# Performance work log

Hardware: AMD Instinct MI355X
Metric: run time of the kernel (lower is better)

Reference implementation:

```python
import jax, jax.numpy as jnp
import numpy as np

CHEB_K = 3


def _cheb(support):
    # Chebyshev polynomial basis [I, A, 2A@T_{k-1} - T_{k-2}] of a dense (N,N) support
    N = support.shape[0]
    ks = [jnp.eye(N, dtype=support.dtype), support]
    for _ in range(2, CHEB_K):
        ks.append(2.0 * support @ ks[-1] - ks[-2])
    return ks


def _agcn(x, sk, W, b):
    # x: (B,N,C); sk: list of (N,N); W: (2*cheb_k*C, O)
    xg = jnp.concatenate([jnp.einsum('nm,bmc->bnc', s, x) for s in sk], axis=-1)
    return jnp.einsum('bni,io->bno', xg, W) + b


def _cell(x, h, sk, Wg, bg, Wu, bu):
    # adaptive graph-conv GRU cell
    hd = h.shape[-1]
    zr = jax.nn.sigmoid(_agcn(jnp.concatenate([x, h], axis=-1), sk, Wg, bg))
    z, r = zr[..., :hd], zr[..., hd:]
    hc = jnp.tanh(_agcn(jnp.concatenate([x, z * h], axis=-1), sk, Wu, bu))
    return r * h + (1.0 - r) * hc


def _forward(x, targets_time, Memory, Wq, We1, We2, egW, egb, euW, eub, dgW, dgb, duW, dub, pW, pb):
    x = jnp.swapaxes(x, 1, -1)  # (B,L,N,C)
    B, L, N, C = x.shape
    H = targets_time.shape[-1]
    ycov = jnp.swapaxes(targets_time, 1, -1)           # (B,H,1,ycov_dim)
    ycov = jnp.broadcast_to(ycov, (B, H, N, ycov.shape[-1]))
    # adaptive adjacency from memory
    e1 = We1 @ Memory
    e2 = We2 @ Memory
    g1 = jax.nn.softmax(jax.nn.relu(e1 @ e2.T), axis=-1)
    g2 = jax.nn.softmax(jax.nn.relu(e2 @ e1.T), axis=-1)
    sk = _cheb(g1) + _cheb(g2)                         # 2*cheb_k supports
    rnn_units = egb.shape[0] // 2
    h0 = jnp.zeros((B, N, rnn_units), x.dtype)
    # encoder: unroll over L (num_layers = 1)
    def enc_step(h, xt):
        return _cell(xt, h, sk, egW, egb, euW, eub), None
    h_t, _ = jax.lax.scan(enc_step, h0, jnp.swapaxes(x, 0, 1))
    # memory attention
    query = h_t @ Wq                                    # (B,N,mem_dim)
    att = jax.nn.softmax(query @ Memory.T, axis=-1)     # (B,N,mem_num)
    h_att = att @ Memory
    h_de = jnp.concatenate([h_t, h_att], axis=-1)       # (B,N,rnn+mem)
    out_dim = pb.shape[0]
    go0 = jnp.zeros((B, N, out_dim), x.dtype)
    def dec_step(carry, yc):
        go, h = carry
        h = _cell(jnp.concatenate([go, yc], axis=-1), h, sk, dgW, dgb, duW, dub)
        go = h @ pW + pb
        return (go, h), go
    _, outs = jax.lax.scan(dec_step, (go0, h_de), jnp.swapaxes(ycov, 0, 1))
    out = jnp.swapaxes(outs, 0, 1)                      # (B,H,N,out_dim)
    return jnp.swapaxes(out, 1, -1)                     # (B,out_dim,N,H)


def setup_inputs() -> dict:
    key = jax.random.key(0)
    ks = jax.random.split(key, 20)
    B, N, L, H = 64, 512, 12, 12
    in_dim, out_dim, ycov_dim = 1, 1, 5
    rnn, mem_num, mem_dim = 64, 20, 64
    dec_dim = rnn + mem_dim
    s = 0.1
    inp = {
        'x': jax.random.normal(ks[0], (B, in_dim, N, L), jnp.float32),
        'adj': jax.random.uniform(ks[1], (N, N), jnp.float32),
        'targets': jax.random.normal(ks[2], (B, out_dim, N, H), jnp.float32),
        'targets_time': jax.random.normal(ks[3], (B, ycov_dim, 1, H), jnp.float32),
        'index': 100,
        'Memory': jax.random.normal(ks[4], (mem_num, mem_dim), jnp.float32) * s,
        'Wq': jax.random.normal(ks[5], (rnn, mem_dim), jnp.float32) * s,
        'We1': jax.random.normal(ks[6], (N, mem_num), jnp.float32) * s,
        'We2': jax.random.normal(ks[7], (N, mem_num), jnp.float32) * s,
        'enc_gate_W': jax.random.normal(ks[8], (2 * CHEB_K * (in_dim + rnn), 2 * rnn), jnp.float32) * s,
        'enc_gate_b': jnp.zeros((2 * rnn,), jnp.float32),
        'enc_upd_W': jax.random.normal(ks[9], (2 * CHEB_K * (in_dim + rnn), rnn), jnp.float32) * s,
        'enc_upd_b': jnp.zeros((rnn,), jnp.float32),
        'dec_gate_W': jax.random.normal(ks[10], (2 * CHEB_K * (out_dim + ycov_dim + dec_dim), 2 * dec_dim), jnp.float32) * s,
        'dec_gate_b': jnp.zeros((2 * dec_dim,), jnp.float32),
        'dec_upd_W': jax.random.normal(ks[11], (2 * CHEB_K * (out_dim + ycov_dim + dec_dim), dec_dim), jnp.float32) * s,
        'dec_upd_b': jnp.zeros((dec_dim,), jnp.float32),
        'proj_W': jax.random.normal(ks[12], (dec_dim, out_dim), jnp.float32) * s,
        'proj_b': jnp.zeros((out_dim,), jnp.float32),
    }
    return inp


def reference(x, adj, targets, targets_time, index, Memory, Wq, We1, We2, enc_gate_W, enc_gate_b, enc_upd_W, enc_upd_b, dec_gate_W, dec_gate_b, dec_upd_W, dec_upd_b, proj_W, proj_b):
    # adj, targets, index only used in training mode; eval path ignores them
    return _forward(x, targets_time, Memory, Wq, We1, We2, enc_gate_W, enc_gate_b, enc_upd_W, enc_upd_b, dec_gate_W, dec_gate_b, dec_upd_W, dec_upd_b, proj_W, proj_b)
```

## Files before the change

### kernel.cpp

```cpp
#include <hip/hip_runtime.h>
#include <hip/hip_bf16.h>
#include <math.h>

typedef __hip_bfloat16 bf16;
typedef __attribute__((ext_vector_type(8))) short s8v;
typedef __attribute__((ext_vector_type(4))) short s4v;
typedef __attribute__((ext_vector_type(4))) float f4v;

#define B_   64
#define N_   512
#define L_   12
#define H_   12
#define RNN  64
#define MEMN 20
#define MEMD 64
#define DD   128
#define NB   32768


__device__ inline void glds16(const bf16* g, bf16* l) {
  __builtin_amdgcn_global_load_lds((const __attribute__((address_space(1))) void*)g,
                                   (__attribute__((address_space(3))) void*)l, 16, 0, 0);
}

__device__ inline int2 xcd_swz() {
  int lid = blockIdx.x + blockIdx.y * gridDim.x;
  int chunk = (gridDim.x * gridDim.y) >> 3;
  int swz = (lid & 7) * chunk + (lid >> 3);
  int bx = swz / gridDim.y;
  int by = swz - bx * gridDim.y;
  return make_int2(bx, by);
}

template<int C_CH, int CP>
__global__ __launch_bounds__(256) void gemm_mix(
    const bf16* __restrict__ Sb, const bf16* __restrict__ XT, bf16* __restrict__ Yb) {
  const int NCOLS = 64 * C_CH;
  __shared__ bf16 As[128 * 32];
  __shared__ bf16 Bs[128 * 32];
  const int tid = threadIdx.x, lane = tid & 63, wid = tid >> 6;
  const int wr = wid >> 1, wc = wid & 1;
  int2 sz = xcd_swz();
  const int bn = sz.x * 128, bm = sz.y * 128;
  const int r_in = lane >> 2, dslot = lane & 3;
  f4v acc[4][4] = {};
  for (int k0 = 0; k0 < 512; k0 += 32) {
#pragma unroll
    for (int h = 0; h < 2; h++) {
      int ci = wid + h * 4;
      int row = ci * 16 + r_in;
      int ss = dslot ^ ((row >> 1) & 3);
      glds16(Sb + (size_t)(bm + row) * 512 + k0 + ss * 8, As + ci * 512);
      glds16(XT + (size_t)(bn + row) * 512 + k0 + ss * 8, Bs + ci * 512);
    }
    asm volatile("s_waitcnt vmcnt(0)" ::: "memory");
    __syncthreads();
    s8v a[4], bb[4];
#pragma unroll
    for (int m = 0; m < 4; m++) {
      int row = wr * 64 + m * 16 + (lane & 15);
      int slot = (lane >> 4) ^ ((row >> 1) & 3);
      a[m] = *(const s8v*)(As + row * 32 + slot * 8);
    }
#pragma unroll
    for (int n = 0; n < 4; n++) {
      int col = wc * 64 + n * 16 + (lane & 15);
      int slot = (lane >> 4) ^ ((col >> 1) & 3);
      bb[n] = *(const s8v*)(Bs + col * 32 + slot * 8);
    }
#pragma unroll
    for (int m = 0; m < 4; m++)
#pragma unroll
      for (int n = 0; n < 4; n++)
        acc[m][n] = __builtin_amdgcn_mfma_f32_16x16x32_bf16(a[m], bb[n], acc[m][n], 0, 0, 0);
    __syncthreads();
  }
#pragma unroll
  for (int m = 0; m < 4; m++) {
#pragma unroll
    for (int rg = 0; rg < 4; rg++) {
      int row = bm + wr * 64 + m * 16 + (lane >> 4) * 4 + rg;
      int s = row >> 9, nn = row & 511;
      size_t obase = (size_t)s * NB * CP;
#pragma unroll
      for (int n = 0; n < 4; n++) {
        int col = bn + wc * 64 + n * 16 + (lane & 15);
        if (col < NCOLS) {
          int b2 = col / C_CH, c = col - b2 * C_CH;
          Yb[obase + (size_t)(b2 * 512 + nn) * CP + c] = __float2bfloat16(acc[m][n][rg]);
        }
      }
    }
  }
}

template<int CP, int OPAD, int EPI, int CCH>
__global__ __launch_bounds__(256) void gemm_proj(
    const bf16* __restrict__ WT, const bf16* __restrict__ XCin,
    const bf16* __restrict__ Yb, const float* __restrict__ bias,
    bf16* __restrict__ RG, float* __restrict__ HT, int hd,
    const float* __restrict__ pW, const float* __restrict__ pb,
    float* __restrict__ outp, bf16* __restrict__ XTo, bf16* __restrict__ XCo,
    bf16* __restrict__ XTa, bf16* __restrict__ XCa, int t) {
  constexpr int MPW = OPAD / 4;
  constexpr int MF  = MPW / 16;
  __shared__ bf16 As[OPAD * 32];
  __shared__ bf16 Bs[64 * 32];
  __shared__ float red2[16 * 64];
  __shared__ float pws[128];
  const int tid = threadIdx.x, lane = tid & 63, wo = tid >> 6;
  int swb = (blockIdx.x & 7) * (gridDim.x >> 3) + (blockIdx.x >> 3);
  const int r0 = swb * 64;
  const int r_in = lane >> 2, dslot = lane & 3;

  if (EPI == 2 && tid < 128) pws[tid] = pW[tid];

  f4v acc[MF][4] = {};
#pragma unroll
  for (int seg = 0; seg < 5; seg++) {
    const bf16* Bbase = (seg == 0) ? XCin : (Yb + (size_t)(seg - 1) * NB * CP);
    const bf16* Abase = WT + (size_t)seg * OPAD * CP;
    for (int k0 = 0; k0 < CP; k0 += 32) {
      for (int ci = wo; ci < OPAD / 16; ci += 4) {
        int row = ci * 16 + r_in;
        int ss = dslot ^ ((row >> 1) & 3);
        glds16(Abase + (size_t)row * CP + k0 + ss * 8, As + ci * 512);
      }
      {
        int row = wo * 16 + r_in;
        int ss = dslot ^ ((row >> 1) & 3);
        glds16(Bbase + (size_t)(r0 + row) * CP + k0 + ss * 8, Bs + wo * 512);
      }
      asm volatile("s_waitcnt vmcnt(0)" ::: "memory");
      __syncthreads();
      s8v a[MF], bb[4];
#pragma unroll
      for (int m = 0; m < MF; m++) {
        int row = wo * MPW + m * 16 + (lane & 15);
        int slot = (lane >> 4) ^ ((row >> 1) & 3);
        a[m] = *(const s8v*)(As + row * 32 + slot * 8);
      }
#pragma unroll
      for (int n = 0; n < 4; n++) {
        int col = n * 16 + (lane & 15);
        int slot = (lane >> 4) ^ ((col >> 1) & 3);
        bb[n] = *(const s8v*)(Bs + col * 32 + slot * 8);
      }
#pragma unroll
      for (int m = 0; m < MF; m++)
#pragma unroll
        for (int n = 0; n < 4; n++)
          acc[m][n] = __builtin_amdgcn_mfma_f32_16x16x32_bf16(a[m], bb[n], acc[m][n], 0, 0, 0);
      __syncthreads();
    }
  }

#pragma unroll
  for (int m = 0; m < MF; m++) {
#pragma unroll
    for (int n = 0; n < 4; n++) {
      int r = r0 + n * 16 + (lane & 15);
      int b2 = r >> 9, nn = r & 511;
      int ch0 = wo * MPW + m * 16 + (lane >> 4) * 4;
      if (EPI == 0) {
        if (ch0 < hd) {
          bf16 z4[4];
#pragma unroll
          for (int rg = 0; rg < 4; rg++) {
            int o = ch0 + rg;
            float sg = 1.f / (1.f + expf(-(acc[m][n][rg] + bias[o])));
            float hold = HT[(size_t)o * NB + r];
            z4[rg] = __float2bfloat16(sg * hold);
            XTo[((size_t)b2 * CCH + o) * 512 + nn] = z4[rg];
          }
          *(s4v*)(XCo + (size_t)r * CP + ch0) = *(const s4v*)z4;
        } else {
#pragma unroll
          for (int rg = 0; rg < 4; rg++) {
            int o = ch0 + rg;
            float sg = 1.f / (1.f + expf(-(acc[m][n][rg] + bias[o])));
            RG[(size_t)(o - hd) * NB + r] = __float2bfloat16(sg);
          }
        }
      } else {
        if (ch0 < hd) {
          bf16 h4[4];
#pragma unroll
          for (int rg = 0; rg < 4; rg++) {
            int o = ch0 + rg;
            float hc = tanhf(acc[m][n][rg] + bias[o]);
            float rgt = __bfloat162float(RG[(size_t)o * NB + r]);
            float* hp = HT + (size_t)o * NB + r;
            float hn = rgt * (*hp) + (1.f - rgt) * hc;
            *hp = hn;
            h4[rg] = __float2bfloat16(hn);
            XTo[((size_t)b2 * CCH + o) * 512 + nn] = h4[rg];
            acc[m][n][rg] = hn;
          }
          *(s4v*)(XCo + (size_t)r * CP + ch0) = *(const s4v*)h4;
        }
      }
    }
  }

  if (EPI == 2) {
    __syncthreads();
#pragma unroll
    for (int n = 0; n < 4; n++) {
      int r_local = n * 16 + (lane & 15);
      float ps = 0.f;
#pragma unroll
      for (int m = 0; m < MF; m++)
#pragma unroll
        for (int rg = 0; rg < 4; rg++) {
          int o = wo * MPW + m * 16 + (lane >> 4) * 4 + rg;
          ps += acc[m][n][rg] * pws[o];
        }
      red2[(wo * 4 + (lane >> 4)) * 64 + r_local] = ps;
    }
    __syncthreads();
    if (tid < 64) {
      float v = pb[0];
#pragma unroll
      for (int s2 = 0; s2 < 16; s2++) v += red2[s2 * 64 + tid];
      int r = r0 + tid;
      int b2 = r >> 9, nn = r & 511;
      outp[b2 * 6144 + nn * 12 + t] = v;
      bf16 gb = __float2bfloat16(v);
      XTo[((size_t)b2 * CCH + hd) * 512 + nn] = gb;
      XCo[(size_t)r * CP + hd] = gb;
      XTa[((size_t)b2 * CCH + hd) * 512 + nn] = gb;
      XCa[(size_t)r * CP + hd] = gb;
    }
  }
}

__global__ __launch_bounds__(256) void gemm_cheb(
    const bf16* __restrict__ A, const bf16* __restrict__ BT, bf16* __restrict__ O) {
  __shared__ bf16 As[128 * 32];
  __shared__ bf16 Bs[128 * 32];
  const int tid = threadIdx.x, lane = tid & 63, wid = tid >> 6;
  const int wr = wid >> 1, wc = wid & 1;
  const int bm = blockIdx.y * 128, bn = blockIdx.x * 128;
  const int r_in = lane >> 2, dslot = lane & 3;
  f4v acc[4][4] = {};
  for (int k0 = 0; k0 < 512; k0 += 32) {
#pragma unroll
    for (int h = 0; h < 2; h++) {
      int ci = wid + h * 4;
      int row = ci * 16 + r_in;
      int ss = dslot ^ ((row >> 1) & 3);
      glds16(A + (size_t)(bm + row) * 512 + k0 + ss * 8, As + ci * 512);
      glds16(BT + (size_t)(bn + row) * 512 + k0 + ss * 8, Bs + ci * 512);
    }
    asm volatile("s_waitcnt vmcnt(0)" ::: "memory");
    __syncthreads();
    s8v a[4], bb[4];
#pragma unroll
    for (int m = 0; m < 4; m++) {
      int row = wr * 64 + m * 16 + (lane & 15);
      int slot = (lane >> 4) ^ ((row >> 1) & 3);
      a[m] = *(const s8v*)(As + row * 32 + slot * 8);
    }
#pragma unroll
    for (int n = 0; n < 4; n++) {
      int col = wc * 64 + n * 16 + (lane & 15);
      int slot = (lane >> 4) ^ ((col >> 1) & 3);
      bb[n] = *(const s8v*)(Bs + col * 32 + slot * 8);
    }
#pragma unroll
    for (int m = 0; m < 4; m++)
#pragma unroll
      for (int n = 0; n < 4; n++)
        acc[m][n] = __builtin_amdgcn_mfma_f32_16x16x32_bf16(a[m], bb[n], acc[m][n], 0, 0, 0);
    __syncthreads();
  }
#pragma unroll
  for (int m = 0; m < 4; m++) {
#pragma unroll
    for (int rg = 0; rg < 4; rg++) {
      int row = bm + wr * 64 + m * 16 + (lane >> 4) * 4 + rg;
#pragma unroll
      for (int n = 0; n < 4; n++) {
        int col = bn + wc * 64 + n * 16 + (lane & 15);
        float v = 2.f * acc[m][n][rg] - (row == col ? 1.f : 0.f);
        O[(size_t)row * 512 + col] = __float2bfloat16(v);
      }
    }
  }
}

__global__ void fill_zero4(float4* p, int n) {
  for (int i = blockIdx.x * 256 + threadIdx.x; i < n; i += gridDim.x * 256)
    p[i] = make_float4(0.f, 0.f, 0.f, 0.f);
}

__global__ void compute_e(const float* __restrict__ We1, const float* __restrict__ We2,
                          const float* __restrict__ Mem, float* __restrict__ e1,
                          float* __restrict__ e2) {
  int idx = blockIdx.x * 256 + threadIdx.x;
  if (idx >= N_ * MEMD) return;
  int n = idx >> 6, d = idx & 63;
  float s1 = 0.f, s2 = 0.f;
  for (int k = 0; k < MEMN; k++) {
    float m = Mem[k * MEMD + d];
    s1 += We1[n * MEMN + k] * m;
    s2 += We2[n * MEMN + k] * m;
  }
  e1[idx] = s1; e2[idx] = s2;
}

__global__ void compute_wqm(const float* __restrict__ Wq, const float* __restrict__ Mem,
                            float* __restrict__ WqM) {
  int idx = blockIdx.x * 256 + threadIdx.x;
  if (idx >= RNN * MEMN) return;
  int c = idx / MEMN, j = idx - c * MEMN;
  float s = 0.f;
  for (int d = 0; d < MEMD; d++) s += Wq[c * MEMD + d] * Mem[j * MEMD + d];
  WqM[idx] = s;
}

__global__ void scores_relu(const float* __restrict__ e1, const float* __restrict__ e2,
                            float* __restrict__ S) {
  int idx = blockIdx.x * 256 + threadIdx.x;
  if (idx >= N_ * N_) return;
  int n = idx >> 9, m = idx & 511;
  float s = 0.f;
  for (int k = 0; k < MEMD; k++) s += e1[n * MEMD + k] * e2[m * MEMD + k];
  S[idx] = s > 0.f ? s : 0.f;
}

__global__ __launch_bounds__(256)
void row_softmax(const float* __restrict__ S, float* __restrict__ G) {
  int r = blockIdx.x;
  __shared__ float red[256];
  float m = -1e30f;
  for (int j = threadIdx.x; j < N_; j += 256) m = fmaxf(m, S[r * N_ + j]);
  red[threadIdx.x] = m; __syncthreads();
  for (int s = 128; s > 0; s >>= 1) {
    if (threadIdx.x < s) red[threadIdx.x] = fmaxf(red[threadIdx.x], red[threadIdx.x + s]);
    __syncthreads();
  }
  m = red[0]; __syncthreads();
  float sum = 0.f;
  for (int j = threadIdx.x; j < N_; j += 256) sum += expf(S[r * N_ + j] - m);
  red[threadIdx.x] = sum; __syncthreads();
  for (int s = 128; s > 0; s >>= 1) {
    if (threadIdx.x < s) red[threadIdx.x] += red[threadIdx.x + s];
    __syncthreads();
  }
  float inv = 1.f / red[0];
  for (int j = threadIdx.x; j < N_; j += 256)
    G[r * N_ + j] = expf(S[r * N_ + j] - m) * inv;
}

__global__ void trans_f32(const float* __restrict__ in, float* __restrict__ outT) {
  __shared__ float t[32][33];
  int bx = blockIdx.x * 32, by = blockIdx.y * 32;
  int x = threadIdx.x, y = threadIdx.y;
  for (int i = 0; i < 32; i += 8) t[y + i][x] = in[(by + y + i) * 512 + bx + x];
  __syncthreads();
  for (int i = 0; i < 32; i += 8) outT[(bx + y + i) * 512 + by + x] = t[x][y + i];
}

__global__ void trans_to_bf16(const float* __restrict__ in, bf16* __restrict__ outN,
                              bf16* __restrict__ outT) {
  __shared__ float t[32][33];
  int bx = blockIdx.x * 32, by = blockIdx.y * 32;
  int x = threadIdx.x, y = threadIdx.y;
  for (int i = 0; i < 32; i += 8) {
    float v = in[(by + y + i) * 512 + bx + x];
    t[y + i][x] = v;
    outN[(by + y + i) * 512 + bx + x] = __float2bfloat16(v);
  }
  __syncthreads();
  for (int i = 0; i < 32; i += 8)
    outT[(bx + y + i) * 512 + by + x] = __float2bfloat16(t[x][y + i]);
}

__global__ void prep_wt(const float* __restrict__ W, bf16* __restrict__ WT,
                        int C, int O, int Opad, int CP, int HD, int MC) {
  int idx = blockIdx.x * 256 + threadIdx.x;
  int tot = 5 * Opad * CP;
  if (idx >= tot) return;
  int seg = idx / (Opad * CP);
  int rem = idx - seg * (Opad * CP);
  int o = rem / CP, c = rem - (rem / CP) * CP;
  float v = 0.f;
  int srcc = -1;
  if (c < HD) srcc = MC + c;
  else if (c < HD + MC) srcc = c - HD;
  if (srcc >= 0 && o < O) {
    const int blkmap[5] = {0, 1, 2, 4, 5};
    int blk = blkmap[seg];
    v = W[(blk * C + srcc) * O + o];
    if (seg == 0) v += W[(3 * C + srcc) * O + o];
  }
  WT[idx] = __float2bfloat16(v);
}

__global__ void fill_misc_enc(bf16* __restrict__ XTh, bf16* __restrict__ XTz,
                              bf16* __restrict__ XCh, bf16* __restrict__ XCz,
                              const float* __restrict__ x, int t) {
  int r = blockIdx.x * 256 + threadIdx.x;
  if (r >= NB) return;
  int b = r >> 9, n = r & 511;
  bf16 v = __float2bfloat16(x[b * 6144 + n * 12 + t]);
  XTh[((size_t)b * 65 + 64) * 512 + n] = v;
  XTz[((size_t)b * 65 + 64) * 512 + n] = v;
  XCh[(size_t)r * 96 + 64] = v;
  XCz[(size_t)r * 96 + 64] = v;
}

__global__ void fill_misc_dec(bf16* __restrict__ XTh, bf16* __restrict__ XTz,
                              bf16* __restrict__ XCh, bf16* __restrict__ XCz,
                              const float* __restrict__ tt, int t, int writego) {
  int idx = blockIdx.x * 256 + threadIdx.x;
  if (idx >= NB * 6) return;
  int ch = idx >> 15, r = idx & (NB - 1);
  int b = r >> 9, n = r & 511;
  bf16 v;
  int c;
  if (ch < 5) { v = __float2bfloat16(tt[b * 60 + ch * 12 + t]); c = 129 + ch; }
  else { if (!writego) return; v = __float2bfloat16(0.f); c = 128; }
  XTh[((size_t)b * 134 + c) * 512 + n] = v;
  XTz[((size_t)b * 134 + c) * 512 + n] = v;
  XCh[(size_t)r * 160 + c] = v;
  XCz[(size_t)r * 160 + c] = v;
}

__global__ __launch_bounds__(128) void attention2(
    const float* __restrict__ HbT, const float* __restrict__ WqM,
    const float* __restrict__ Mem, float* __restrict__ HdT,
    bf16* __restrict__ XTh, bf16* __restrict__ XCh) {
  __shared__ float h[64][128];
  __shared__ float wqm[64][20];
  __shared__ float mem[20][64];
  const int tid = threadIdx.x, r0 = blockIdx.x * 128;
  const int r = r0 + tid, b = r >> 9, n = r & 511;
  for (int e = tid; e < 64 * 128; e += 128) {
    int c = e >> 7, j = e & 127;
    h[c][j] = HbT[(size_t)c * NB + r0 + j];
  }
  for (int e = tid; e < 1280; e += 128) {
    wqm[e / 20][e % 20] = WqM[e];
    mem[e >> 6][e & 63] = Mem[e];
  }
  __syncthreads();
  float s[20];
#pragma unroll
  for (int j = 0; j < 20; j++) s[j] = 0.f;
  for (int c = 0; c < 64; c++) {
    float hv = h[c][tid];
#pragma unroll
    for (int j = 0; j < 20; j++) s[j] += hv * wqm[c][j];
  }
  float mx = s[0];
#pragma unroll
  for (int j = 1; j < 20; j++) mx = fmaxf(mx, s[j]);
  float sum = 0.f;
#pragma unroll
  for (int j = 0; j < 20; j++) { s[j] = expf(s[j] - mx); sum += s[j]; }
  float inv = 1.f / sum;
#pragma unroll
  for (int j = 0; j < 20; j++) s[j] *= inv;
  for (int d = 0; d < 64; d++) {
    float ha = 0.f;
#pragma unroll
    for (int j = 0; j < 20; j++) ha += s[j] * mem[j][d];
    float hv = h[d][tid];
    HdT[(size_t)d * NB + r] = hv;
    HdT[(size_t)(64 + d) * NB + r] = ha;
    bf16 hb = __float2bfloat16(hv), ab = __float2bfloat16(ha);
    XTh[((size_t)b * 134 + d) * 512 + n] = hb;
    XTh[((size_t)b * 134 + 64 + d) * 512 + n] = ab;
    XCh[(size_t)r * 160 + d] = hb;
    XCh[(size_t)r * 160 + 64 + d] = ab;
  }
}

extern "C" void kernel_launch(void* const* d_in, const int* in_sizes, int n_in,
                              void* d_out, int out_size, void* d_ws, size_t ws_size,
                              hipStream_t stream) {
  const float* x   = (const float*)d_in[0];
  const float* tt  = (const float*)d_in[3];
  const float* Mem = (const float*)d_in[5];
  const float* Wq  = (const float*)d_in[6];
  const float* We1 = (const float*)d_in[7];
  const float* We2 = (const float*)d_in[8];
  const float* egW = (const float*)d_in[9];
  const float* egb = (const float*)d_in[10];
  const float* euW = (const float*)d_in[11];
  const float* eub = (const float*)d_in[12];
  const float* dgW = (const float*)d_in[13];
  const float* dgb = (const float*)d_in[14];
  const float* duW = (const float*)d_in[15];
  const float* dub = (const float*)d_in[16];
  const float* pW  = (const float*)d_in[17];
  const float* pb  = (const float*)d_in[18];
  float* out = (float*)d_out;

  char* ws = (char*)d_ws;
  size_t off = 0;
  auto alloc = [&](size_t bytes) { char* p = ws + off; off += (bytes + 255) & ~(size_t)255; return p; };
  bf16* XTh   = (bf16*)alloc((size_t)8576 * 512 * 2);
  bf16* XCh   = (bf16*)alloc((size_t)NB * 160 * 2);
  float* HbT  = (float*)alloc((size_t)RNN * NB * 4);
  size_t zero_bytes = off;
  bf16* XTz   = (bf16*)alloc((size_t)8576 * 512 * 2);
  bf16* XCz   = (bf16*)alloc((size_t)NB * 160 * 2);
  bf16* Ybuf  = (bf16*)alloc((size_t)4 * NB * 160 * 2);
  bf16* RG    = (bf16*)alloc((size_t)DD * NB * 2);
  bf16* WTeg  = (bf16*)alloc((size_t)5 * 128 * 96 * 2);
  bf16* WTeu  = (bf16*)alloc((size_t)5 * 64 * 96 * 2);
  bf16* WTdg  = (bf16*)alloc((size_t)5 * 256 * 160 * 2);
  bf16* WTdu  = (bf16*)alloc((size_t)5 * 128 * 160 * 2);
  bf16* Sb    = (bf16*)alloc((size_t)4 * 512 * 512 * 2);
  bf16* g1T   = (bf16*)alloc((size_t)512 * 512 * 2);
  bf16* g2T   = (bf16*)alloc((size_t)512 * 512 * 2);
  float* HdT  = (float*)alloc((size_t)DD * NB * 4);
  float* WqM  = (float*)alloc((size_t)RNN * MEMN * 4);
  float* e1   = (float*)alloc((size_t)N_ * MEMD * 4);
  float* e2   = (float*)alloc((size_t)N_ * MEMD * 4);
  float* S    = (float*)alloc((size_t)N_ * N_ * 4);
  float* ST   = (float*)alloc((size_t)N_ * N_ * 4);
  float* g1f  = (float*)alloc((size_t)N_ * N_ * 4);
  float* g2f  = (float*)alloc((size_t)N_ * N_ * 4);

  auto blk = [](long n) { return dim3((unsigned)((n + 255) / 256)); };

  fill_zero4<<<2048, 256, 0, stream>>>((float4*)ws, (int)(zero_bytes / 16));
  compute_e<<<blk(N_ * MEMD), 256, 0, stream>>>(We1, We2, Mem, e1, e2);
  compute_wqm<<<blk(RNN * MEMN), 256, 0, stream>>>(Wq, Mem, WqM);
  scores_relu<<<blk(N_ * N_), 256, 0, stream>>>(e1, e2, S);
  trans_f32<<<dim3(16, 16), dim3(32, 8), 0, stream>>>(S, ST);
  row_softmax<<<N_, 256, 0, stream>>>(S, g1f);
  row_softmax<<<N_, 256, 0, stream>>>(ST, g2f);
  trans_to_bf16<<<dim3(16, 16), dim3(32, 8), 0, stream>>>(g1f, Sb + 0 * 262144, g1T);
  trans_to_bf16<<<dim3(16, 16), dim3(32, 8), 0, stream>>>(g2f, Sb + 2 * 262144, g2T);
  gemm_cheb<<<dim3(4, 4), 256, 0, stream>>>(Sb + 0 * 262144, g1T, Sb + 1 * 262144);
  gemm_cheb<<<dim3(4, 4), 256, 0, stream>>>(Sb + 2 * 262144, g2T, Sb + 3 * 262144);
  prep_wt<<<blk(5 * 128 * 96), 256, 0, stream>>>(egW, WTeg, 65, 128, 128, 96, 64, 1);
  prep_wt<<<blk(5 * 64 * 96), 256, 0, stream>>>(euW, WTeu, 65, 64, 64, 96, 64, 1);
  prep_wt<<<blk(5 * 256 * 160), 256, 0, stream>>>(dgW, WTdg, 134, 256, 256, 160, 128, 6);
  prep_wt<<<blk(5 * 128 * 160), 256, 0, stream>>>(duW, WTdu, 134, 128, 128, 160, 128, 6);

  for (int t = 0; t < L_; t++) {
    fill_misc_enc<<<blk(NB), 256, 0, stream>>>(XTh, XTz, XCh, XCz, x, t);
    gemm_mix<65, 96><<<dim3(33, 16), 256, 0, stream>>>(Sb, XTh, Ybuf);
    gemm_proj<96, 128, 0, 65><<<512, 256, 0, stream>>>(
        WTeg, XCh, Ybuf, egb, RG, HbT, RNN, nullptr, nullptr, nullptr,
        XTz, XCz, nullptr, nullptr, 0);
    gemm_mix<65, 96><<<dim3(33, 16), 256, 0, stream>>>(Sb, XTz, Ybuf);
    gemm_proj<96, 64, 1, 65><<<512, 256, 0, stream>>>(
        WTeu, XCz, Ybuf, eub, RG, HbT, RNN, nullptr, nullptr, nullptr,
        XTh, XCh, nullptr, nullptr, 0);
  }

  attention2<<<dim3(256), 128, 0, stream>>>(HbT, WqM, Mem, HdT, XTh, XCh);

  for (int t = 0; t < H_; t++) {
    fill_misc_dec<<<blk((long)NB * 6), 256, 0, stream>>>(XTh, XTz, XCh, XCz, tt, t, t == 0);
    gemm_mix<134, 160><<<dim3(67, 16), 256, 0, stream>>>(Sb, XTh, Ybuf);
    gemm_proj<160, 256, 0, 134><<<512, 256, 0, stream>>>(
        WTdg, XCh, Ybuf, dgb, RG, HdT, DD, nullptr, nullptr, nullptr,
        XTz, XCz, nullptr, nullptr, 0);
    gemm_mix<134, 160><<<dim3(67, 16), 256, 0, stream>>>(Sb, XTz, Ybuf);
    gemm_proj<160, 128, 2, 134><<<512, 256, 0, stream>>>(
        WTdu, XCz, Ybuf, dub, RG, HdT, DD, pW, pb, out,
        XTh, XCh, XTz, XCz, t);
  }
}
```

Before: 2.602 ms.

## Halve gemm_proj row tile and fuse next-step input fill into epilogue

The projection GEMM's row tile is halved from 64 to 32 rows per block, doubling the grid to 1024 blocks to improve occupancy and CU utilization. The per-timestep fill_misc_enc/fill_misc_dec launches are removed from the loops. The next step's x and time-covariate channels are instead written in the update-gate epilogue, saving a kernel launch and a pass over memory each step. The smaller tile reloads the weight tile more often per output row, raising A-operand traffic.

```diff
diff --git a/kernel.cpp b/kernel.cpp
--- a/kernel.cpp
+++ b/kernel.cpp
@@ -101,21 +101,22 @@
     bf16* __restrict__ RG, float* __restrict__ HT, int hd,
     const float* __restrict__ pW, const float* __restrict__ pb,
     float* __restrict__ outp, bf16* __restrict__ XTo, bf16* __restrict__ XCo,
-    bf16* __restrict__ XTa, bf16* __restrict__ XCa, int t) {
+    bf16* __restrict__ XTa, bf16* __restrict__ XCa, int t,
+    const float* __restrict__ msrc, int tnext) {
   constexpr int MPW = OPAD / 4;
   constexpr int MF  = MPW / 16;
   __shared__ bf16 As[OPAD * 32];
-  __shared__ bf16 Bs[64 * 32];
-  __shared__ float red2[16 * 64];
+  __shared__ bf16 Bs[32 * 32];
+  __shared__ float red2[16 * 32];
   __shared__ float pws[128];
   const int tid = threadIdx.x, lane = tid & 63, wo = tid >> 6;
   int swb = (blockIdx.x & 7) * (gridDim.x >> 3) + (blockIdx.x >> 3);
-  const int r0 = swb * 64;
+  const int r0 = swb * 32;
   const int r_in = lane >> 2, dslot = lane & 3;
 
   if (EPI == 2 && tid < 128) pws[tid] = pW[tid];
 
-  f4v acc[MF][4] = {};
+  f4v acc[MF][2] = {};
 #pragma unroll
   for (int seg = 0; seg < 5; seg++) {
     const bf16* Bbase = (seg == 0) ? XCin : (Yb + (size_t)(seg - 1) * NB * CP);
@@ -126,14 +127,14 @@
         int ss = dslot ^ ((row >> 1) & 3);
         glds16(Abase + (size_t)row * CP + k0 + ss * 8, As + ci * 512);
       }
-      {
+      if (wo < 2) {
         int row = wo * 16 + r_in;
         int ss = dslot ^ ((row >> 1) & 3);
         glds16(Bbase + (size_t)(r0 + row) * CP + k0 + ss * 8, Bs + wo * 512);
       }
       asm volatile("s_waitcnt vmcnt(0)" ::: "memory");
       __syncthreads();
-      s8v a[MF], bb[4];
+      s8v a[MF], bb[2];
 #pragma unroll
       for (int m = 0; m < MF; m++) {
         int row = wo * MPW + m * 16 + (lane & 15);
@@ -141,7 +142,7 @@
         a[m] = *(const s8v*)(As + row * 32 + slot * 8);
       }
 #pragma unroll
-      for (int n = 0; n < 4; n++) {
+      for (int n = 0; n < 2; n++) {
         int col = n * 16 + (lane & 15);
         int slot = (lane >> 4) ^ ((col >> 1) & 3);
         bb[n] = *(const s8v*)(Bs + col * 32 + slot * 8);
@@ -149,7 +150,7 @@
 #pragma unroll
       for (int m = 0; m < MF; m++)
 #pragma unroll
-        for (int n = 0; n < 4; n++)
+        for (int n = 0; n < 2; n++)
           acc[m][n] = __builtin_amdgcn_mfma_f32_16x16x32_bf16(a[m], bb[n], acc[m][n], 0, 0, 0);
       __syncthreads();
     }
@@ -158,7 +159,7 @@
 #pragma unroll
   for (int m = 0; m < MF; m++) {
 #pragma unroll
-    for (int n = 0; n < 4; n++) {
+    for (int n = 0; n < 2; n++) {
       int r = r0 + n * 16 + (lane & 15);
       int b2 = r >> 9, nn = r & 511;
       int ch0 = wo * MPW + m * 16 + (lane >> 4) * 4;
@@ -203,10 +204,20 @@
     }
   }
 
+  if (EPI == 1 && msrc != nullptr && tnext < L_ && tid < 32) {
+    int r = r0 + tid;
+    int b2 = r >> 9, nn = r & 511;
+    bf16 v = __float2bfloat16(msrc[b2 * 6144 + nn * 12 + tnext]);
+    XTo[((size_t)b2 * CCH + hd) * 512 + nn] = v;
+    XCo[(size_t)r * CP + hd] = v;
+    XTa[((size_t)b2 * CCH + hd) * 512 + nn] = v;
+    XCa[(size_t)r * CP + hd] = v;
+  }
+
   if (EPI == 2) {
     __syncthreads();
 #pragma unroll
-    for (int n = 0; n < 4; n++) {
+    for (int n = 0; n < 2; n++) {
       int r_local = n * 16 + (lane & 15);
       float ps = 0.f;
 #pragma unroll
@@ -216,13 +227,13 @@
           int o = wo * MPW + m * 16 + (lane >> 4) * 4 + rg;
           ps += acc[m][n][rg] * pws[o];
         }
-      red2[(wo * 4 + (lane >> 4)) * 64 + r_local] = ps;
-    }
-    __syncthreads();
-    if (tid < 64) {
+      red2[(wo * 4 + (lane >> 4)) * 32 + r_local] = ps;
+    }
+    __syncthreads();
+    if (tid < 32) {
       float v = pb[0];
 #pragma unroll
-      for (int s2 = 0; s2 < 16; s2++) v += red2[s2 * 64 + tid];
+      for (int s2 = 0; s2 < 16; s2++) v += red2[s2 * 32 + tid];
       int r = r0 + tid;
       int b2 = r >> 9, nn = r & 511;
       outp[b2 * 6144 + nn * 12 + t] = v;
@@ -231,6 +242,17 @@
       XCo[(size_t)r * CP + hd] = gb;
       XTa[((size_t)b2 * CCH + hd) * 512 + nn] = gb;
       XCa[(size_t)r * CP + hd] = gb;
+      if (msrc != nullptr && tnext < H_) {
+#pragma unroll
+        for (int ch = 0; ch < 5; ch++) {
+          bf16 tv = __float2bfloat16(msrc[b2 * 60 + ch * 12 + tnext]);
+          int c = hd + 1 + ch;
+          XTo[((size_t)b2 * CCH + c) * 512 + nn] = tv;
+          XCo[(size_t)r * CP + c] = tv;
+          XTa[((size_t)b2 * CCH + c) * 512 + nn] = tv;
+          XCa[(size_t)r * CP + c] = tv;
+        }
+      }
     }
   }
 }
@@ -545,29 +567,29 @@
   prep_wt<<<blk(5 * 256 * 160), 256, 0, stream>>>(dgW, WTdg, 134, 256, 256, 160, 128, 6);
   prep_wt<<<blk(5 * 128 * 160), 256, 0, stream>>>(duW, WTdu, 134, 128, 128, 160, 128, 6);
 
+  fill_misc_enc<<<blk(NB), 256, 0, stream>>>(XTh, XTz, XCh, XCz, x, 0);
   for (int t = 0; t < L_; t++) {
-    fill_misc_enc<<<blk(NB), 256, 0, stream>>>(XTh, XTz, XCh, XCz, x, t);
     gemm_mix<65, 96><<<dim3(33, 16), 256, 0, stream>>>(Sb, XTh, Ybuf);
-    gemm_proj<96, 128, 0, 65><<<512, 256, 0, stream>>>(
+    gemm_proj<96, 128, 0, 65><<<1024, 256, 0, stream>>>(
         WTeg, XCh, Ybuf, egb, RG, HbT, RNN, nullptr, nullptr, nullptr,
-        XTz, XCz, nullptr, nullptr, 0);
+        XTz, XCz, nullptr, nullptr, 0, nullptr, 99);
     gemm_mix<65, 96><<<dim3(33, 16), 256, 0, stream>>>(Sb, XTz, Ybuf);
-    gemm_proj<96, 64, 1, 65><<<512, 256, 0, stream>>>(
+    gemm_proj<96, 64, 1, 65><<<1024, 256, 0, stream>>>(
         WTeu, XCz, Ybuf, eub, RG, HbT, RNN, nullptr, nullptr, nullptr,
-        XTh, XCh, nullptr, nullptr, 0);
+        XTh, XCh, XTz, XCz, 0, x, t + 1);
   }
 
   attention2<<<dim3(256), 128, 0, stream>>>(HbT, WqM, Mem, HdT, XTh, XCh);
 
+  fill_misc_dec<<<blk((long)NB * 6), 256, 0, stream>>>(XTh, XTz, XCh, XCz, tt, 0, 1);
   for (int t = 0; t < H_; t++) {
-    fill_misc_dec<<<blk((long)NB * 6), 256, 0, stream>>>(XTh, XTz, XCh, XCz, tt, t, t == 0);
     gemm_mix<134, 160><<<dim3(67, 16), 256, 0, stream>>>(Sb, XTh, Ybuf);
-    gemm_proj<160, 256, 0, 134><<<512, 256, 0, stream>>>(
+    gemm_proj<160, 256, 0, 134><<<1024, 256, 0, stream>>>(
         WTdg, XCh, Ybuf, dgb, RG, HdT, DD, nullptr, nullptr, nullptr,
-        XTz, XCz, nullptr, nullptr, 0);
+        XTz, XCz, nullptr, nullptr, 0, nullptr, 99);
     gemm_mix<134, 160><<<dim3(67, 16), 256, 0, stream>>>(Sb, XTz, Ybuf);
-    gemm_proj<160, 128, 2, 134><<<512, 256, 0, stream>>>(
+    gemm_proj<160, 128, 2, 134><<<1024, 256, 0, stream>>>(
         WTdu, XCz, Ybuf, dub, RG, HdT, DD, pW, pb, out,
-        XTh, XCh, XTz, XCz, t);
-  }
-}
+        XTh, XCh, XTz, XCz, t, tt, t + 1);
+  }
+}
```

Result: faster. 2.550 ms (median of 13 runs) (-2.0%).
